# Kernel tuning notes

Measured on AMD Instinct MI355X. Metric: run time of the kernel, lower is better.

Reference implementation:

```python
import jax, jax.numpy as jnp
import numpy as np

B, C, H, W = 32, 512, 24, 8
C8 = C // 8  # PAM query/key channels


def setup_inputs() -> dict:
    key = jax.random.key(0)
    k0, k1, k2, k3, k4 = jax.random.split(key, 5)
    x = jax.random.normal(k0, (B, C, H, W), dtype=jnp.float32)
    Wq = jax.random.normal(k1, (C8, C), dtype=jnp.float32) * 0.02
    bq = jnp.zeros((C8,), dtype=jnp.float32)
    Wk = jax.random.normal(k2, (C8, C), dtype=jnp.float32) * 0.02
    bk = jnp.zeros((C8,), dtype=jnp.float32)
    return {"x": x, "Wq": Wq, "bq": bq, "Wk": Wk, "bk": bk}


def reference(x, Wq, bq, Wk, bk):
    b, c, h, w = x.shape
    hw = h * w
    xf = x.reshape(b, c, hw)  # [B, C, hw]

    # QAConv: einsum('gchw,pcyx->gpyxhw') with kernel == x, then view(B,-1,hw,hw).
    # With m=(h,w) of features and n=(y,x) of kernel this is 'gcm,pcn->gpnm'.
    score = jnp.einsum('gcm,pcn->gpnm', xf, xf)  # [B, B, hw, hw]
    kernel_max = score.max(axis=3)               # max over feature positions -> [B, B, hw]

    # PAM: 1x1 conv projections then bmm(q^T, k).
    q = jnp.einsum('qc,bcm->bqm', Wq, xf) + bq[None, :, None]  # [B, C8, hw]
    k = jnp.einsum('qc,bcm->bqm', Wk, xf) + bk[None, :, None]  # [B, C8, hw]
    energy = jnp.einsum('bqm,bqn->bmn', q, k)                  # [B, hw, hw]
    pos_max = energy.max(axis=2)[None]                         # [1, B, hw]

    return jnp.concatenate([kernel_max, pos_max], axis=0)  # [B+1, B, hw]
```

## Files before the change

### kernel.cpp

```cpp
#include <hip/hip_runtime.h>

typedef __bf16 bf16x8 __attribute__((ext_vector_type(8)));
typedef float f32x4 __attribute__((ext_vector_type(4)));
typedef unsigned short u16x8 __attribute__((ext_vector_type(8)));
typedef unsigned short u16x4 __attribute__((ext_vector_type(4)));

#define B_ 32
#define CC 512
#define HW 192
#define C8_ 64
#define NTRI 528
#define TILE_B 24576
#define SMEM_BYTES 102912

__device__ inline unsigned short f2bf(float f) {
    unsigned u = __float_as_uint(f);
    unsigned r = (u + 0x7FFFu + ((u >> 16) & 1u)) >> 16;
    return (unsigned short)r;
}

__device__ inline void gload16(const void* g, void* l) {
    __builtin_amdgcn_global_load_lds(
        (const __attribute__((address_space(1))) unsigned*)g,
        (__attribute__((address_space(3))) unsigned*)l,
        16, 0, 0);
}

__global__ void k_transpose(const float* __restrict__ x,
                            unsigned short* __restrict__ xt) {
    __shared__ unsigned short tile[64 * 64];
    int b = blockIdx.x / 3, mt = blockIdx.x % 3;
    int m0 = mt * 64, c0 = blockIdx.y * 64;
    int t = threadIdx.x;
    const float* xb = x + (size_t)b * CC * HW + (size_t)c0 * HW + m0;

    int mq = t & 15, cl0 = t >> 4;
    int sw = (mq & 7) << 3;
    #pragma unroll
    for (int rd = 0; rd < 4; ++rd) {
        int cl = rd * 16 + cl0;
        f32x4 v = *(const f32x4*)(xb + cl * HW + mq * 4);
        #pragma unroll
        for (int e = 0; e < 4; ++e)
            tile[(mq * 4 + e) * 64 + (cl ^ sw)] = f2bf(v[e]);
    }
    __syncthreads();
    unsigned short* xo = xt + ((size_t)b * HW + m0) * CC + c0;
    int kc = t & 7, mr0 = t >> 3;
    #pragma unroll
    for (int rd = 0; rd < 2; ++rd) {
        int mr = rd * 32 + mr0;
        u16x8 v = *(const u16x8*)&tile[mr * 64 + ((kc << 3) ^ (((mr >> 2) & 7) << 3))];
        *(u16x8*)(xo + (size_t)mr * CC + kc * 8) = v;
    }
}

__global__ void wcvt(const float* __restrict__ Wq, const float* __restrict__ Wk,
                     unsigned short* __restrict__ wqb, unsigned short* __restrict__ wkb) {
    const float* src = (blockIdx.x < 32) ? Wq : Wk;
    unsigned short* dst = (blockIdx.x < 32) ? wqb : wkb;
    int base = (blockIdx.x & 31) * 1024 + threadIdx.x * 4;
    f32x4 a = *(const f32x4*)(src + base);
    u16x4 o;
    #pragma unroll
    for (int e = 0; e < 4; ++e) o[e] = f2bf(a[e]);
    *(u16x4*)(dst + base) = o;
}

__global__ __launch_bounds__(256) void pam_qk(
        const unsigned short* __restrict__ xt,
        const unsigned short* __restrict__ wqb, const unsigned short* __restrict__ wkb,
        const float* __restrict__ bq, const float* __restrict__ bk,
        unsigned short* __restrict__ qo, unsigned short* __restrict__ ko) {
    int b = blockIdx.x, m0 = blockIdx.y * 48;
    int tid = threadIdx.x, w = tid >> 6, lane = tid & 63;
    int l15 = lane & 15, lq = lane >> 4;
    int qc = w * 16 + l15;

    f32x4 accq[3], acck[3];
    #pragma unroll
    for (int i = 0; i < 3; ++i) {
        accq[i] = (f32x4){0.f, 0.f, 0.f, 0.f};
        acck[i] = (f32x4){0.f, 0.f, 0.f, 0.f};
    }

    const unsigned short* xb = xt + ((size_t)b * HW + m0) * CC;
    const unsigned short* wqp = wqb + (size_t)qc * CC;
    const unsigned short* wkp = wkb + (size_t)qc * CC;

    for (int kt = 0; kt < 16; ++kt) {
        int ko8 = kt * 32 + lq * 8;
        bf16x8 wqf = *(const bf16x8*)(wqp + ko8);
        bf16x8 wkf = *(const bf16x8*)(wkp + ko8);
        bf16x8 af[3];
        #pragma unroll
        for (int i = 0; i < 3; ++i)
            af[i] = *(const bf16x8*)(xb + (i * 16 + l15) * CC + ko8);
        #pragma unroll
        for (int i = 0; i < 3; ++i) {
            accq[i] = __builtin_amdgcn_mfma_f32_16x16x32_bf16(af[i], wqf, accq[i], 0, 0, 0);
            acck[i] = __builtin_amdgcn_mfma_f32_16x16x32_bf16(af[i], wkf, acck[i], 0, 0, 0);
        }
    }

    float bqv = bq[qc], bkv = bk[qc];
    #pragma unroll
    for (int i = 0; i < 3; ++i) {
        #pragma unroll
        for (int r = 0; r < 4; ++r) {
            int m = m0 + i * 16 + lq * 4 + r;
            qo[((size_t)b * HW + m) * C8_ + qc] = f2bf(accq[i][r] + bqv);
            ko[((size_t)b * HW + m) * C8_ + qc] = f2bf(acck[i][r] + bkv);
        }
    }
}

__global__ __launch_bounds__(256) void pam_energy(
        const unsigned short* __restrict__ qo,
        const unsigned short* __restrict__ ko,
        float* __restrict__ out) {
    int b = blockIdx.x, m0 = blockIdx.y * 48;
    int tid = threadIdx.x, w = tid >> 6, lane = tid & 63;
    int l15 = lane & 15, lq = lane >> 4;
    int n0 = w * 48;

    f32x4 acc[3][3];
    #pragma unroll
    for (int i = 0; i < 3; ++i)
        #pragma unroll
        for (int j = 0; j < 3; ++j)
            acc[i][j] = (f32x4){0.f, 0.f, 0.f, 0.f};

    const unsigned short* qb = qo + ((size_t)b * HW + m0) * C8_;
    const unsigned short* kb = ko + ((size_t)b * HW + n0) * C8_;

    #pragma unroll
    for (int kt = 0; kt < 2; ++kt) {
        int ko8 = kt * 32 + lq * 8;
        bf16x8 af[3], bfr[3];
        #pragma unroll
        for (int i = 0; i < 3; ++i)
            af[i] = *(const bf16x8*)(qb + (i * 16 + l15) * C8_ + ko8);
        #pragma unroll
        for (int j = 0; j < 3; ++j)
            bfr[j] = *(const bf16x8*)(kb + (j * 16 + l15) * C8_ + ko8);
        #pragma unroll
        for (int i = 0; i < 3; ++i)
            #pragma unroll
            for (int j = 0; j < 3; ++j)
                acc[i][j] = __builtin_amdgcn_mfma_f32_16x16x32_bf16(af[i], bfr[j], acc[i][j], 0, 0, 0);
    }

    __shared__ float red[4][48];
    #pragma unroll
    for (int i = 0; i < 3; ++i) {
        float rm[4];
        #pragma unroll
        for (int r = 0; r < 4; ++r) rm[r] = -1e30f;
        #pragma unroll
        for (int j = 0; j < 3; ++j)
            #pragma unroll
            for (int r = 0; r < 4; ++r)
                rm[r] = fmaxf(rm[r], acc[i][j][r]);
        #pragma unroll
        for (int msk = 1; msk <= 8; msk <<= 1)
            #pragma unroll
            for (int r = 0; r < 4; ++r)
                rm[r] = fmaxf(rm[r], __shfl_xor(rm[r], msk));
        if (l15 == 0) {
            #pragma unroll
            for (int r = 0; r < 4; ++r)
                red[w][i * 16 + lq * 4 + r] = rm[r];
        }
    }
    __syncthreads();
    if (tid < 48) {
        float v = fmaxf(fmaxf(red[0][tid], red[1][tid]),
                        fmaxf(red[2][tid], red[3][tid]));
        out[((size_t)B_ * B_ + b) * HW + m0 + tid] = v;
    }
}

__global__ __launch_bounds__(512) void gram(const unsigned short* __restrict__ xt,
                                            float* __restrict__ out) {
    extern __shared__ char smem[];
    float* colbuf = (float*)(smem + 2 * TILE_B * 2);
    float* rowbuf = (float*)(smem + 2 * TILE_B * 2 + 1536);

    int tid = threadIdx.x;
    int bid = (blockIdx.x & 7) * 66 + (blockIdx.x >> 3);
    int idx = bid, g = 0;
    while (idx >= B_ - g) { idx -= B_ - g; ++g; }
    int p = g + idx;

    const unsigned short* xg = xt + (size_t)g * HW * CC;
    const unsigned short* xp = xt + (size_t)p * HW * CC;

    int w = tid >> 6, lane = tid & 63;
    int wr = w >> 2, wc = w & 3;
    int l15 = lane & 15, lq = lane >> 4;

    int l8 = lane >> 3, s8 = lane & 7;
    const unsigned short* agp = xg + (size_t)(24 * w + l8) * CC + ((s8 ^ l8) << 3);
    const unsigned short* bgp = xp + (size_t)(24 * w + l8) * CC + ((s8 ^ l8) << 3);
    unsigned ldsw = (unsigned)(24 * w) * 128;

    unsigned aoff[6], boff[3];
    #pragma unroll
    for (int i = 0; i < 6; ++i) {
        int row = wr * 96 + i * 16 + l15;
        aoff[i] = row * 128 + ((unsigned)(lq ^ (row & 7)) << 4);
    }
    #pragma unroll
    for (int j = 0; j < 3; ++j) {
        int row = wc * 48 + j * 16 + l15;
        boff[j] = row * 128 + ((unsigned)(lq ^ (row & 7)) << 4);
    }

    f32x4 acc[6][3];
    #pragma unroll
    for (int i = 0; i < 6; ++i)
        #pragma unroll
        for (int j = 0; j < 3; ++j)
            acc[i][j] = (f32x4){0.f, 0.f, 0.f, 0.f};

    #define STAGE(buf, k0)                                                     \
        {                                                                      \
            char* ab = smem + (buf) * TILE_B + ldsw;                           \
            char* bb = smem + 2 * TILE_B + (buf) * TILE_B + ldsw;              \
            _Pragma("unroll")                                                  \
            for (int ci = 0; ci < 3; ++ci) {                                   \
                gload16(agp + (k0) + ci * 8 * CC, ab + ci * 1024);             \
                gload16(bgp + (k0) + ci * 8 * CC, bb + ci * 1024);             \
            }                                                                  \
        }

    STAGE(0, 0);
    __syncthreads();

    for (int kt = 0; kt < 8; ++kt) {
        int cur = kt & 1;
        if (kt < 7) STAGE(cur ^ 1, (kt + 1) * 64);
        const char* Ab = smem + cur * TILE_B;
        const char* Bb = smem + 2 * TILE_B + cur * TILE_B;
        #pragma unroll
        for (int kx = 0; kx < 128; kx += 64) {
            bf16x8 af[6], bfr[3];
            #pragma unroll
            for (int i = 0; i < 6; ++i)
                af[i] = *(const bf16x8*)(Ab + (aoff[i] ^ kx));
            #pragma unroll
            for (int j = 0; j < 3; ++j)
                bfr[j] = *(const bf16x8*)(Bb + (boff[j] ^ kx));
            #pragma unroll
            for (int i = 0; i < 6; ++i)
                #pragma unroll
                for (int j = 0; j < 3; ++j)
                    acc[i][j] = __builtin_amdgcn_mfma_f32_16x16x32_bf16(
                        af[i], bfr[j], acc[i][j], 0, 0, 0);
        }
        __syncthreads();
    }

    #pragma unroll
    for (int j = 0; j < 3; ++j) {
        float cm = -1e30f;
        #pragma unroll
        for (int i = 0; i < 6; ++i)
            #pragma unroll
            for (int r = 0; r < 4; ++r)
                cm = fmaxf(cm, acc[i][j][r]);
        cm = fmaxf(cm, __shfl_xor(cm, 16));
        cm = fmaxf(cm, __shfl_xor(cm, 32));
        if (lane < 16) colbuf[wr * HW + wc * 48 + j * 16 + l15] = cm;
    }
    #pragma unroll
    for (int i = 0; i < 6; ++i) {
        float rm[4];
        #pragma unroll
        for (int r = 0; r < 4; ++r) rm[r] = -1e30f;
        #pragma unroll
        for (int j = 0; j < 3; ++j)
            #pragma unroll
            for (int r = 0; r < 4; ++r)
                rm[r] = fmaxf(rm[r], acc[i][j][r]);
        #pragma unroll
        for (int msk = 1; msk <= 8; msk <<= 1)
            #pragma unroll
            for (int r = 0; r < 4; ++r)
                rm[r] = fmaxf(rm[r], __shfl_xor(rm[r], msk));
        if (l15 == 0) {
            #pragma unroll
            for (int r = 0; r < 4; ++r)
                rowbuf[wc * HW + wr * 96 + i * 16 + lq * 4 + r] = rm[r];
        }
    }
    __syncthreads();
    if (tid < HW) {
        float cmax = fmaxf(colbuf[tid], colbuf[HW + tid]);
        out[((size_t)g * B_ + p) * HW + tid] = cmax;
        float rmax = fmaxf(fmaxf(rowbuf[tid], rowbuf[HW + tid]),
                           fmaxf(rowbuf[2 * HW + tid], rowbuf[3 * HW + tid]));
        out[((size_t)p * B_ + g) * HW + tid] = rmax;
    }
}

extern "C" void kernel_launch(void* const* d_in, const int* in_sizes, int n_in,
                              void* d_out, int out_size, void* d_ws, size_t ws_size,
                              hipStream_t stream) {
    (void)in_sizes; (void)n_in; (void)out_size; (void)ws_size;
    const float* x  = (const float*)d_in[0];
    const float* Wq = (const float*)d_in[1];
    const float* bq = (const float*)d_in[2];
    const float* Wk = (const float*)d_in[3];
    const float* bk = (const float*)d_in[4];
    float* out = (float*)d_out;

    char* ws = (char*)d_ws;
    unsigned short* xt  = (unsigned short*)ws;
    unsigned short* wqb = (unsigned short*)(ws + 6291456);
    unsigned short* wkb = (unsigned short*)(ws + 6291456 + 65536);
    unsigned short* qbuf = (unsigned short*)(ws + 6291456 + 131072);
    unsigned short* kbuf = (unsigned short*)(ws + 6291456 + 131072 + 786432);

    hipFuncSetAttribute((const void*)gram,
                        hipFuncAttributeMaxDynamicSharedMemorySize, SMEM_BYTES);

    k_transpose<<<dim3(96, 8), dim3(256), 0, stream>>>(x, xt);
    wcvt<<<dim3(64), dim3(256), 0, stream>>>(Wq, Wk, wqb, wkb);
    pam_qk<<<dim3(32, 4), dim3(256), 0, stream>>>(xt, wqb, wkb, bq, bk, qbuf, kbuf);
    pam_energy<<<dim3(32, 4), dim3(256), 0, stream>>>(qbuf, kbuf, out);
    gram<<<dim3(NTRI), dim3(512), SMEM_BYTES, stream>>>(xt, out);
}
```

Baseline: 62.42 us.

## Triple-buffer gram kernel K-loop with explicit vmcnt waits and single barrier

Replaces the double-buffered K loop in the gram kernel with a fully unrolled triple-buffered pipeline. Two stages are prefetched ahead, and each step waits with a partial s_waitcnt vmcnt(6) plus one barrier instead of a full __syncthreads after compute. The aim is to overlap more global-to-LDS load latency with MFMA work and drop one barrier per iteration. LDS use grows from about 100KB to about 150KB per block, and correctness now depends on the hand-written vmcnt counts matching the number of issued loads.

```diff
diff --git a/kernel.cpp b/kernel.cpp
--- a/kernel.cpp
+++ b/kernel.cpp
@@ -11,7 +11,7 @@
 #define C8_ 64
 #define NTRI 528
 #define TILE_B 24576
-#define SMEM_BYTES 102912
+#define SMEM_BYTES 152064
 
 __device__ inline unsigned short f2bf(float f) {
     unsigned u = __float_as_uint(f);
@@ -184,8 +184,8 @@
 __global__ __launch_bounds__(512) void gram(const unsigned short* __restrict__ xt,
                                             float* __restrict__ out) {
     extern __shared__ char smem[];
-    float* colbuf = (float*)(smem + 2 * TILE_B * 2);
-    float* rowbuf = (float*)(smem + 2 * TILE_B * 2 + 1536);
+    float* colbuf = (float*)(smem + 6 * TILE_B);
+    float* rowbuf = (float*)(smem + 6 * TILE_B + 1536);
 
     int tid = threadIdx.x;
     int bid = (blockIdx.x & 7) * 66 + (blockIdx.x >> 3);
@@ -226,8 +226,8 @@
 
     #define STAGE(buf, k0)                                                     \
         {                                                                      \
-            char* ab = smem + (buf) * TILE_B + ldsw;                           \
-            char* bb = smem + 2 * TILE_B + (buf) * TILE_B + ldsw;              \
+            char* ab = smem + (buf) * (2 * TILE_B) + ldsw;                     \
+            char* bb = ab + TILE_B;                                            \
             _Pragma("unroll")                                                  \
             for (int ci = 0; ci < 3; ++ci) {                                   \
                 gload16(agp + (k0) + ci * 8 * CC, ab + ci * 1024);             \
@@ -235,32 +235,43 @@
             }                                                                  \
         }
 
+    #define COMPUTE(buf)                                                       \
+        {                                                                      \
+            const char* Ab = smem + (buf) * (2 * TILE_B);                      \
+            const char* Bb = Ab + TILE_B;                                      \
+            _Pragma("unroll")                                                  \
+            for (int kx = 0; kx < 128; kx += 64) {                             \
+                bf16x8 af[6], bfr[3];                                          \
+                _Pragma("unroll")                                              \
+                for (int i = 0; i < 6; ++i)                                    \
+                    af[i] = *(const bf16x8*)(Ab + (aoff[i] ^ kx));             \
+                _Pragma("unroll")                                              \
+                for (int j = 0; j < 3; ++j)                                    \
+                    bfr[j] = *(const bf16x8*)(Bb + (boff[j] ^ kx));            \
+                _Pragma("unroll")                                              \
+                for (int i = 0; i < 6; ++i)                                    \
+                    _Pragma("unroll")                                          \
+                    for (int j = 0; j < 3; ++j)                                \
+                        acc[i][j] = __builtin_amdgcn_mfma_f32_16x16x32_bf16(   \
+                            af[i], bfr[j], acc[i][j], 0, 0, 0);                \
+            }                                                                  \
+        }
+
+    #define WAIT6() asm volatile("s_waitcnt vmcnt(6)" ::: "memory")
+    #define WAIT0() asm volatile("s_waitcnt vmcnt(0)" ::: "memory")
+    #define BAR()   { __builtin_amdgcn_sched_barrier(0); __builtin_amdgcn_s_barrier(); }
+
     STAGE(0, 0);
-    __syncthreads();
-
-    for (int kt = 0; kt < 8; ++kt) {
-        int cur = kt & 1;
-        if (kt < 7) STAGE(cur ^ 1, (kt + 1) * 64);
-        const char* Ab = smem + cur * TILE_B;
-        const char* Bb = smem + 2 * TILE_B + cur * TILE_B;
-        #pragma unroll
-        for (int kx = 0; kx < 128; kx += 64) {
-            bf16x8 af[6], bfr[3];
-            #pragma unroll
-            for (int i = 0; i < 6; ++i)
-                af[i] = *(const bf16x8*)(Ab + (aoff[i] ^ kx));
-            #pragma unroll
-            for (int j = 0; j < 3; ++j)
-                bfr[j] = *(const bf16x8*)(Bb + (boff[j] ^ kx));
-            #pragma unroll
-            for (int i = 0; i < 6; ++i)
-                #pragma unroll
-                for (int j = 0; j < 3; ++j)
-                    acc[i][j] = __builtin_amdgcn_mfma_f32_16x16x32_bf16(
-                        af[i], bfr[j], acc[i][j], 0, 0, 0);
-        }
-        __syncthreads();
-    }
+    STAGE(1, 64);
+
+    WAIT6(); BAR(); STAGE(2, 2 * 64); COMPUTE(0);
+    WAIT6(); BAR(); STAGE(0, 3 * 64); COMPUTE(1);
+    WAIT6(); BAR(); STAGE(1, 4 * 64); COMPUTE(2);
+    WAIT6(); BAR(); STAGE(2, 5 * 64); COMPUTE(0);
+    WAIT6(); BAR(); STAGE(0, 6 * 64); COMPUTE(1);
+    WAIT6(); BAR(); STAGE(1, 7 * 64); COMPUTE(2);
+    WAIT6(); BAR();                   COMPUTE(0);
+    WAIT0(); BAR();                   COMPUTE(1);
 
     #pragma unroll
     for (int j = 0; j < 3; ++j) {
```

Measured after the change: 63.98 us. +2.5%, slower.

## Triple-buffer gram K-loop with smaller K-tiles and explicit vmcnt waits

Applied to the files above, without the earlier changes.

Restructures the gram kernel's K-loop from double-buffered 64-wide K tiles to triple-buffered 32-wide tiles. Each wave loads either A or B rows, and explicit s_waitcnt vmcnt with a raw barrier replaces __syncthreads, so two stages stay in flight. Shared memory per block drops and launch bounds request 4 blocks per CU to raise occupancy. The tradeoff is more barriers per K element and a new LDS swizzle, plus register pressure from the occupancy hint, which could cause spills.

```diff
diff --git a/kernel.cpp b/kernel.cpp
--- a/kernel.cpp
+++ b/kernel.cpp
@@ -10,8 +10,8 @@
 #define HW 192
 #define C8_ 64
 #define NTRI 528
-#define TILE_B 24576
-#define SMEM_BYTES 102912
+#define PAIR_B 24576
+#define SMEM_BYTES 73728
 
 __device__ inline unsigned short f2bf(float f) {
     unsigned u = __float_as_uint(f);
@@ -181,11 +181,9 @@
     }
 }
 
-__global__ __launch_bounds__(512) void gram(const unsigned short* __restrict__ xt,
-                                            float* __restrict__ out) {
+__global__ __launch_bounds__(512, 4) void gram(const unsigned short* __restrict__ xt,
+                                               float* __restrict__ out) {
     extern __shared__ char smem[];
-    float* colbuf = (float*)(smem + 2 * TILE_B * 2);
-    float* rowbuf = (float*)(smem + 2 * TILE_B * 2 + 1536);
 
     int tid = threadIdx.x;
     int bid = (blockIdx.x & 7) * 66 + (blockIdx.x >> 3);
@@ -200,22 +198,20 @@
     int wr = w >> 2, wc = w & 3;
     int l15 = lane & 15, lq = lane >> 4;
 
-    int l8 = lane >> 3, s8 = lane & 7;
-    const unsigned short* agp = xg + (size_t)(24 * w + l8) * CC + ((s8 ^ l8) << 3);
-    const unsigned short* bgp = xp + (size_t)(24 * w + l8) * CC + ((s8 ^ l8) << 3);
-    unsigned ldsw = (unsigned)(24 * w) * 128;
-
+    int rowbase = (w & 3) * 48;
+    const unsigned short* gsrc = (w < 4 ? xg : xp)
+        + (size_t)(rowbase + (lane >> 2)) * CC
+        + (((lane & 3) ^ ((lane >> 3) & 3)) << 3);
+    unsigned ldsoff = (unsigned)(w < 4 ? 0 : 12288) + (unsigned)rowbase * 64;
+
+    unsigned ssw = (unsigned)((lq ^ ((l15 >> 1) & 3)) << 4);
     unsigned aoff[6], boff[3];
     #pragma unroll
-    for (int i = 0; i < 6; ++i) {
-        int row = wr * 96 + i * 16 + l15;
-        aoff[i] = row * 128 + ((unsigned)(lq ^ (row & 7)) << 4);
-    }
-    #pragma unroll
-    for (int j = 0; j < 3; ++j) {
-        int row = wc * 48 + j * 16 + l15;
-        boff[j] = row * 128 + ((unsigned)(lq ^ (row & 7)) << 4);
-    }
+    for (int i = 0; i < 6; ++i)
+        aoff[i] = (unsigned)(wr * 96 + i * 16 + l15) * 64 + ssw;
+    #pragma unroll
+    for (int j = 0; j < 3; ++j)
+        boff[j] = 12288u + (unsigned)(wc * 48 + j * 16 + l15) * 64 + ssw;
 
     f32x4 acc[6][3];
     #pragma unroll
@@ -224,44 +220,50 @@
         for (int j = 0; j < 3; ++j)
             acc[i][j] = (f32x4){0.f, 0.f, 0.f, 0.f};
 
-    #define STAGE(buf, k0)                                                     \
+    #define STAGE(buf, kt)                                                     \
         {                                                                      \
-            char* ab = smem + (buf) * TILE_B + ldsw;                           \
-            char* bb = smem + 2 * TILE_B + (buf) * TILE_B + ldsw;              \
+            char* db = smem + (buf) * PAIR_B + ldsoff;                         \
+            const unsigned short* gp = gsrc + (kt) * 32;                       \
             _Pragma("unroll")                                                  \
-            for (int ci = 0; ci < 3; ++ci) {                                   \
-                gload16(agp + (k0) + ci * 8 * CC, ab + ci * 1024);             \
-                gload16(bgp + (k0) + ci * 8 * CC, bb + ci * 1024);             \
-            }                                                                  \
-        }
+            for (int ci = 0; ci < 3; ++ci)                                     \
+                gload16(gp + ci * 16 * CC, db + ci * 1024);                    \
+        }
+
+    #define COMPUTE(buf)                                                       \
+        {                                                                      \
+            const char* Bb = smem + (buf) * PAIR_B;                            \
+            bf16x8 af[6], bfr[3];                                              \
+            _Pragma("unroll")                                                  \
+            for (int i = 0; i < 6; ++i)                                        \
+                af[i] = *(const bf16x8*)(Bb + aoff[i]);                        \
+            _Pragma("unroll")                                                  \
+            for (int j = 0; j < 3; ++j)                                        \
+                bfr[j] = *(const bf16x8*)(Bb + boff[j]);                       \
+            _Pragma("unroll")                                                  \
+            for (int i = 0; i < 6; ++i)                                        \
+                _Pragma("unroll")                                              \
+                for (int j = 0; j < 3; ++j)                                    \
+                    acc[i][j] = __builtin_amdgcn_mfma_f32_16x16x32_bf16(       \
+                        af[i], bfr[j], acc[i][j], 0, 0, 0);                    \
+        }
+
+    #define WAIT3() asm volatile("s_waitcnt vmcnt(3)" ::: "memory")
+    #define WAIT0() asm volatile("s_waitcnt vmcnt(0)" ::: "memory")
+    #define BAR()   { __builtin_amdgcn_sched_barrier(0); __builtin_amdgcn_s_barrier(); }
 
     STAGE(0, 0);
-    __syncthreads();
-
-    for (int kt = 0; kt < 8; ++kt) {
-        int cur = kt & 1;
-        if (kt < 7) STAGE(cur ^ 1, (kt + 1) * 64);
-        const char* Ab = smem + cur * TILE_B;
-        const char* Bb = smem + 2 * TILE_B + cur * TILE_B;
-        #pragma unroll
-        for (int kx = 0; kx < 128; kx += 64) {
-            bf16x8 af[6], bfr[3];
-            #pragma unroll
-            for (int i = 0; i < 6; ++i)
-                af[i] = *(const bf16x8*)(Ab + (aoff[i] ^ kx));
-            #pragma unroll
-            for (int j = 0; j < 3; ++j)
-                bfr[j] = *(const bf16x8*)(Bb + (boff[j] ^ kx));
-            #pragma unroll
-            for (int i = 0; i < 6; ++i)
-                #pragma unroll
-                for (int j = 0; j < 3; ++j)
-                    acc[i][j] = __builtin_amdgcn_mfma_f32_16x16x32_bf16(
-                        af[i], bfr[j], acc[i][j], 0, 0, 0);
-        }
-        __syncthreads();
-    }
-
+    STAGE(1, 1);
+
+    #pragma unroll
+    for (int kt = 0; kt < 16; ++kt) {
+        if (kt < 15) { WAIT3(); } else { WAIT0(); }
+        BAR();
+        if (kt < 14) STAGE((kt + 2) % 3, kt + 2);
+        COMPUTE(kt % 3);
+    }
+
+    float* colbuf = (float*)(smem + PAIR_B);
+    float* rowbuf = colbuf + 2 * HW;
     #pragma unroll
     for (int j = 0; j < 3; ++j) {
         float cm = -1e30f;
```

Result: faster. 60.33 us (-3.3%).

## Retile gram kernel to 4 waves with 96x96 warp tiles and fuse prep kernels

Applied to the files above, without the earlier changes.

The gram kernel drops from 512 threads with 96x48 per-wave tiles to 256 threads with 96x96 per-wave tiles. It uses a smaller k-step of 32 with double-buffered 48KB static LDS, a new swizzle, and launch bounds targeting two blocks per CU. The transpose and weight-convert kernels are merged into a single prep launch, and gram is launched before pam_energy. The intent is to raise MFMA-per-LDS-read reuse and cut launch overhead. The cost is more accumulator registers per wave and twice as many k-iterations and barriers.

```diff
diff --git a/kernel.cpp b/kernel.cpp
--- a/kernel.cpp
+++ b/kernel.cpp
@@ -10,8 +10,7 @@
 #define HW 192
 #define C8_ 64
 #define NTRI 528
-#define TILE_B 24576
-#define SMEM_BYTES 102912
+#define FBUF_B 24576
 
 __device__ inline unsigned short f2bf(float f) {
     unsigned u = __float_as_uint(f);
@@ -26,12 +25,26 @@
         16, 0, 0);
 }
 
-__global__ void k_transpose(const float* __restrict__ x,
-                            unsigned short* __restrict__ xt) {
+__global__ void prep(const float* __restrict__ x,
+                     const float* __restrict__ Wq, const float* __restrict__ Wk,
+                     unsigned short* __restrict__ xt,
+                     unsigned short* __restrict__ wqb, unsigned short* __restrict__ wkb) {
     __shared__ unsigned short tile[64 * 64];
+    int t = threadIdx.x;
+    if (blockIdx.x >= 96) {
+        int id = (blockIdx.x - 96) * 8 + blockIdx.y;
+        const float* src = (id < 32) ? Wq : Wk;
+        unsigned short* dst = (id < 32) ? wqb : wkb;
+        int base = (id & 31) * 1024 + t * 4;
+        f32x4 a = *(const f32x4*)(src + base);
+        u16x4 o;
+        #pragma unroll
+        for (int e = 0; e < 4; ++e) o[e] = f2bf(a[e]);
+        *(u16x4*)(dst + base) = o;
+        return;
+    }
     int b = blockIdx.x / 3, mt = blockIdx.x % 3;
     int m0 = mt * 64, c0 = blockIdx.y * 64;
-    int t = threadIdx.x;
     const float* xb = x + (size_t)b * CC * HW + (size_t)c0 * HW + m0;
 
     int mq = t & 15, cl0 = t >> 4;
@@ -53,18 +66,6 @@
         u16x8 v = *(const u16x8*)&tile[mr * 64 + ((kc << 3) ^ (((mr >> 2) & 7) << 3))];
         *(u16x8*)(xo + (size_t)mr * CC + kc * 8) = v;
     }
-}
-
-__global__ void wcvt(const float* __restrict__ Wq, const float* __restrict__ Wk,
-                     unsigned short* __restrict__ wqb, unsigned short* __restrict__ wkb) {
-    const float* src = (blockIdx.x < 32) ? Wq : Wk;
-    unsigned short* dst = (blockIdx.x < 32) ? wqb : wkb;
-    int base = (blockIdx.x & 31) * 1024 + threadIdx.x * 4;
-    f32x4 a = *(const f32x4*)(src + base);
-    u16x4 o;
-    #pragma unroll
-    for (int e = 0; e < 4; ++e) o[e] = f2bf(a[e]);
-    *(u16x4*)(dst + base) = o;
 }
 
 __global__ __launch_bounds__(256) void pam_qk(
@@ -115,6 +116,130 @@
     }
 }
 
+__global__ __launch_bounds__(256, 2) void gram5(const unsigned short* __restrict__ xt,
+                                                float* __restrict__ out) {
+    __shared__ __attribute__((aligned(16))) char smem[2 * FBUF_B];
+
+    int tid = threadIdx.x;
+    int bid = (blockIdx.x & 7) * 66 + (blockIdx.x >> 3);
+    int idx = bid, g = 0;
+    while (idx >= B_ - g) { idx -= B_ - g; ++g; }
+    int p = g + idx;
+
+    const unsigned short* xg = xt + (size_t)g * HW * CC;
+    const unsigned short* xp = xt + (size_t)p * HW * CC;
+
+    int w = tid >> 6, lane = tid & 63;
+    int wr = w >> 1, wc = w & 1;
+    int l15 = lane & 15, lq = lane >> 4;
+
+    int sc = ((tid & 3) ^ ((tid >> 3) & 3)) << 3;
+    const unsigned short* baseA = xg + (size_t)(tid >> 2) * CC + sc;
+    const unsigned short* baseB = xp + (size_t)(tid >> 2) * CC + sc;
+    unsigned ldsA = (unsigned)tid * 16;
+
+    unsigned aoff[6], boff[6];
+    #pragma unroll
+    for (int i = 0; i < 6; ++i) {
+        int row = wr * 96 + i * 16 + l15;
+        aoff[i] = (unsigned)row * 64 + ((unsigned)(lq ^ ((row >> 1) & 3)) << 4);
+    }
+    #pragma unroll
+    for (int j = 0; j < 6; ++j) {
+        int n = wc * 96 + j * 16 + l15;
+        boff[j] = 12288u + (unsigned)n * 64 + ((unsigned)(lq ^ ((n >> 1) & 3)) << 4);
+    }
+
+    f32x4 acc[6][6];
+    #pragma unroll
+    for (int i = 0; i < 6; ++i)
+        #pragma unroll
+        for (int j = 0; j < 6; ++j)
+            acc[i][j] = (f32x4){0.f, 0.f, 0.f, 0.f};
+
+    #define STG5(buf, kt)                                                      \
+        {                                                                      \
+            char* base = smem + (buf) * FBUF_B;                                \
+            int k0 = (kt) * 32;                                                \
+            _Pragma("unroll")                                                  \
+            for (int ci = 0; ci < 3; ++ci) {                                   \
+                gload16(baseA + k0 + ci * 64 * CC, base + ldsA + ci * 4096);   \
+                gload16(baseB + k0 + ci * 64 * CC,                             \
+                        base + 12288 + ldsA + ci * 4096);                      \
+            }                                                                  \
+        }
+
+    #define CMP5(buf)                                                          \
+        {                                                                      \
+            const char* Bb = smem + (buf) * FBUF_B;                            \
+            bf16x8 bfr[6];                                                     \
+            _Pragma("unroll")                                                  \
+            for (int j = 0; j < 6; ++j)                                        \
+                bfr[j] = *(const bf16x8*)(Bb + boff[j]);                       \
+            _Pragma("unroll")                                                  \
+            for (int i = 0; i < 6; ++i) {                                      \
+                bf16x8 a = *(const bf16x8*)(Bb + aoff[i]);                     \
+                _Pragma("unroll")                                              \
+                for (int j = 0; j < 6; ++j)                                    \
+                    acc[i][j] = __builtin_amdgcn_mfma_f32_16x16x32_bf16(       \
+                        a, bfr[j], acc[i][j], 0, 0, 0);                        \
+            }                                                                  \
+        }
+
+    STG5(0, 0);
+    __syncthreads();
+    for (int kt = 0; kt < 16; ++kt) {
+        int cur = kt & 1;
+        if (kt < 15) STG5(cur ^ 1, kt + 1);
+        CMP5(cur);
+        __syncthreads();
+    }
+
+    float* colbuf = (float*)smem;
+    float* rowbuf = (float*)(smem + 1536);
+
+    #pragma unroll
+    for (int i = 0; i < 6; ++i) {
+        float rm[4];
+        #pragma unroll
+        for (int r = 0; r < 4; ++r) rm[r] = -1e30f;
+        #pragma unroll
+        for (int j = 0; j < 6; ++j)
+            #pragma unroll
+            for (int r = 0; r < 4; ++r)
+                rm[r] = fmaxf(rm[r], acc[i][j][r]);
+        #pragma unroll
+        for (int msk = 1; msk <= 8; msk <<= 1)
+            #pragma unroll
+            for (int r = 0; r < 4; ++r)
+                rm[r] = fmaxf(rm[r], __shfl_xor(rm[r], msk));
+        if (l15 == 0) {
+            #pragma unroll
+            for (int r = 0; r < 4; ++r)
+                rowbuf[wc * HW + wr * 96 + i * 16 + lq * 4 + r] = rm[r];
+        }
+    }
+    #pragma unroll
+    for (int j = 0; j < 6; ++j) {
+        float cm = -1e30f;
+        #pragma unroll
+        for (int i = 0; i < 6; ++i)
+            #pragma unroll
+            for (int r = 0; r < 4; ++r)
+                cm = fmaxf(cm, acc[i][j][r]);
+        cm = fmaxf(cm, __shfl_xor(cm, 16));
+        cm = fmaxf(cm, __shfl_xor(cm, 32));
+        if (lane < 16) colbuf[wr * HW + wc * 96 + j * 16 + l15] = cm;
+    }
+    __syncthreads();
+    if (tid < HW) {
+        float cmax = fmaxf(colbuf[tid], colbuf[HW + tid]);
+        out[((size_t)g * B_ + p) * HW + tid] = cmax;
+        float rmax = fmaxf(rowbuf[tid], rowbuf[HW + tid]);
+        out[((size_t)p * B_ + g) * HW + tid] = rmax;
+    }
+}
+
 __global__ __launch_bounds__(256) void pam_energy(
         const unsigned short* __restrict__ qo,
         const unsigned short* __restrict__ ko,
@@ -178,130 +303,6 @@
         float v = fmaxf(fmaxf(red[0][tid], red[1][tid]),
                         fmaxf(red[2][tid], red[3][tid]));
         out[((size_t)B_ * B_ + b) * HW + m0 + tid] = v;
-    }
-}
-
-__global__ __launch_bounds__(512) void gram(const unsigned short* __restrict__ xt,
-                                            float* __restrict__ out) {
-    extern __shared__ char smem[];
-    float* colbuf = (float*)(smem + 2 * TILE_B * 2);
-    float* rowbuf = (float*)(smem + 2 * TILE_B * 2 + 1536);
-
-    int tid = threadIdx.x;
-    int bid = (blockIdx.x & 7) * 66 + (blockIdx.x >> 3);
-    int idx = bid, g = 0;
-    while (idx >= B_ - g) { idx -= B_ - g; ++g; }
-    int p = g + idx;
-
-    const unsigned short* xg = xt + (size_t)g * HW * CC;
-    const unsigned short* xp = xt + (size_t)p * HW * CC;
-
-    int w = tid >> 6, lane = tid & 63;
-    int wr = w >> 2, wc = w & 3;
-    int l15 = lane & 15, lq = lane >> 4;
-
-    int l8 = lane >> 3, s8 = lane & 7;
-    const unsigned short* agp = xg + (size_t)(24 * w + l8) * CC + ((s8 ^ l8) << 3);
-    const unsigned short* bgp = xp + (size_t)(24 * w + l8) * CC + ((s8 ^ l8) << 3);
-    unsigned ldsw = (unsigned)(24 * w) * 128;
-
-    unsigned aoff[6], boff[3];
-    #pragma unroll
-    for (int i = 0; i < 6; ++i) {
-        int row = wr * 96 + i * 16 + l15;
-        aoff[i] = row * 128 + ((unsigned)(lq ^ (row & 7)) << 4);
-    }
-    #pragma unroll
-    for (int j = 0; j < 3; ++j) {
-        int row = wc * 48 + j * 16 + l15;
-        boff[j] = row * 128 + ((unsigned)(lq ^ (row & 7)) << 4);
-    }
-
-    f32x4 acc[6][3];
-    #pragma unroll
-    for (int i = 0; i < 6; ++i)
-        #pragma unroll
-        for (int j = 0; j < 3; ++j)
-            acc[i][j] = (f32x4){0.f, 0.f, 0.f, 0.f};
-
-    #define STAGE(buf, k0)                                                     \
-        {                                                                      \
-            char* ab = smem + (buf) * TILE_B + ldsw;                           \
-            char* bb = smem + 2 * TILE_B + (buf) * TILE_B + ldsw;              \
-            _Pragma("unroll")                                                  \
-            for (int ci = 0; ci < 3; ++ci) {                                   \
-                gload16(agp + (k0) + ci * 8 * CC, ab + ci * 1024);             \
-                gload16(bgp + (k0) + ci * 8 * CC, bb + ci * 1024);             \
-            }                                                                  \
-        }
-
-    STAGE(0, 0);
-    __syncthreads();
-
-    for (int kt = 0; kt < 8; ++kt) {
-        int cur = kt & 1;
-        if (kt < 7) STAGE(cur ^ 1, (kt + 1) * 64);
-        const char* Ab = smem + cur * TILE_B;
-        const char* Bb = smem + 2 * TILE_B + cur * TILE_B;
-        #pragma unroll
-        for (int kx = 0; kx < 128; kx += 64) {
-            bf16x8 af[6], bfr[3];
-            #pragma unroll
-            for (int i = 0; i < 6; ++i)
-                af[i] = *(const bf16x8*)(Ab + (aoff[i] ^ kx));
-            #pragma unroll
-            for (int j = 0; j < 3; ++j)
-                bfr[j] = *(const bf16x8*)(Bb + (boff[j] ^ kx));
-            #pragma unroll
-            for (int i = 0; i < 6; ++i)
-                #pragma unroll
-                for (int j = 0; j < 3; ++j)
-                    acc[i][j] = __builtin_amdgcn_mfma_f32_16x16x32_bf16(
-                        af[i], bfr[j], acc[i][j], 0, 0, 0);
-        }
-        __syncthreads();
-    }
-
-    #pragma unroll
-    for (int j = 0; j < 3; ++j) {
-        float cm = -1e30f;
-        #pragma unroll
-        for (int i = 0; i < 6; ++i)
-            #pragma unroll
-            for (int r = 0; r < 4; ++r)
-                cm = fmaxf(cm, acc[i][j][r]);
-        cm = fmaxf(cm, __shfl_xor(cm, 16));
-        cm = fmaxf(cm, __shfl_xor(cm, 32));
-        if (lane < 16) colbuf[wr * HW + wc * 48 + j * 16 + l15] = cm;
-    }
-    #pragma unroll
-    for (int i = 0; i < 6; ++i) {
-        float rm[4];
-        #pragma unroll
-        for (int r = 0; r < 4; ++r) rm[r] = -1e30f;
-        #pragma unroll
-        for (int j = 0; j < 3; ++j)
-            #pragma unroll
-            for (int r = 0; r < 4; ++r)
-                rm[r] = fmaxf(rm[r], acc[i][j][r]);
-        #pragma unroll
-        for (int msk = 1; msk <= 8; msk <<= 1)
-            #pragma unroll
-            for (int r = 0; r < 4; ++r)
-                rm[r] = fmaxf(rm[r], __shfl_xor(rm[r], msk));
-        if (l15 == 0) {
-            #pragma unroll
-            for (int r = 0; r < 4; ++r)
-                rowbuf[wc * HW + wr * 96 + i * 16 + lq * 4 + r] = rm[r];
-        }
-    }
-    __syncthreads();
-    if (tid < HW) {
-        float cmax = fmaxf(colbuf[tid], colbuf[HW + tid]);
-        out[((size_t)g * B_ + p) * HW + tid] = cmax;
-        float rmax = fmaxf(fmaxf(rowbuf[tid], rowbuf[HW + tid]),
-                           fmaxf(rowbuf[2 * HW + tid], rowbuf[3 * HW + tid]));
-        out[((size_t)p * B_ + g) * HW + tid] = rmax;
     }
 }
 
@@ -323,12 +324,8 @@
     unsigned short* qbuf = (unsigned short*)(ws + 6291456 + 131072);
     unsigned short* kbuf = (unsigned short*)(ws + 6291456 + 131072 + 786432);
 
-    hipFuncSetAttribute((const void*)gram,
-                        hipFuncAttributeMaxDynamicSharedMemorySize, SMEM_BYTES);
-
-    k_transpose<<<dim3(96, 8), dim3(256), 0, stream>>>(x, xt);
-    wcvt<<<dim3(64), dim3(256), 0, stream>>>(Wq, Wk, wqb, wkb);
+    prep<<<dim3(104, 8), dim3(256), 0, stream>>>(x, Wq, Wk, xt, wqb, wkb);
     pam_qk<<<dim3(32, 4), dim3(256), 0, stream>>>(xt, wqb, wkb, bq, bk, qbuf, kbuf);
+    gram5<<<dim3(NTRI), dim3(256), 0, stream>>>(xt, out);
     pam_energy<<<dim3(32, 4), dim3(256), 0, stream>>>(qbuf, kbuf, out);
-    gram<<<dim3(NTRI), dim3(512), SMEM_BYTES, stream>>>(xt, out);
-}
+}
```

Result: faster. 58.42 us (-6.4%).
